# Kernel tuning notes

Measured on AMD Instinct MI355X. Metric: run time of the kernel, lower is better.

Reference implementation:

```python
import jax, jax.numpy as jnp
import numpy as np

N = 32768          # flattened tokens
D = 256            # latent_dim
K = 8192           # codebook_size
COMMIT_W = 0.25    # commitment_weight


def setup_inputs() -> dict:
    key = jax.random.key(0)
    k1, k2, k3 = jax.random.split(key, 3)
    x = jax.random.normal(k1, (N, D), dtype=jnp.float32)
    # nn.init.uniform_(embedding.weight, -1/K, 1/K)
    embedding = jax.random.uniform(k2, (K, D), dtype=jnp.float32,
                                   minval=-1.0 / K, maxval=1.0 / K)
    # out_proj: Linear(D, D, bias=False); torch default kaiming-uniform ~ U(-1/sqrt(D), 1/sqrt(D))
    lim = 1.0 / np.sqrt(D)
    w_out = jax.random.uniform(k3, (D, D), dtype=jnp.float32, minval=-lim, maxval=lim)
    return {"x": x, "embedding": embedding, "w_out": w_out}


def reference(x, embedding, w_out):
    sg = jax.lax.stop_gradient
    # codebook = out_proj(embedding.weight)  -> [K, D]
    codebook = embedding @ w_out.T
    # torch.cdist(x, codebook, p=2) is only consumed by argmin, so squared
    # Euclidean distances give the identical ids without the sqrt.
    x2 = jnp.sum(x * x, axis=1, keepdims=True)          # [N, 1]
    c2 = jnp.sum(codebook * codebook, axis=1)           # [K]
    dists = x2 - 2.0 * (x @ codebook.T) + c2            # [N, K]
    ids = jnp.argmin(dists, axis=1)                     # [N]
    q = codebook[ids]                                   # [N, D] gather
    # straight-through estimator
    quantized = x + sg(q - x)
    loss = jnp.mean((x - sg(quantized)) ** 2) \
         + COMMIT_W * jnp.mean((quantized - sg(x)) ** 2)
    return quantized, ids, loss
```

## Files before the change

kernel.cpp:

```cpp
#include <hip/hip_runtime.h>
#include <hip/hip_bf16.h>

#define N_TOK 32768
#define DIM   256
#define KCB   8192
#define CAP   64
#define MARGIN 1.75e-4f

typedef __attribute__((ext_vector_type(8))) short short8v;
typedef __attribute__((ext_vector_type(4))) float f32x4;

__device__ __forceinline__ unsigned int mono_f32(float f) {
    unsigned int u = __float_as_uint(f);
    return (u >> 31) ? ~u : (u | 0x80000000u);
}
__device__ __forceinline__ float invmono_f32(unsigned int m) {
    unsigned int u = (m & 0x80000000u) ? (m & 0x7FFFFFFFu) : ~m;
    return __uint_as_float(u);
}
__device__ __forceinline__ unsigned long long shfl_xor_u64(unsigned long long v, int m) {
    unsigned int lo = (unsigned int)v, hi = (unsigned int)(v >> 32);
    lo = __shfl_xor(lo, m, 64);
    hi = __shfl_xor(hi, m, 64);
    return ((unsigned long long)hi << 32) | lo;
}
__device__ __forceinline__ void gl_lds16(const void* g, void* l) {
    __builtin_amdgcn_global_load_lds(
        (const __attribute__((address_space(1))) unsigned int*)g,
        (__attribute__((address_space(3))) unsigned int*)l, 16, 0, 0);
}
__device__ __forceinline__ unsigned int rne16(float f) {
    unsigned int b = __float_as_uint(f);
    return (b + 0x7FFFu + ((b >> 16) & 1u)) >> 16;
}

__global__ __launch_bounds__(256) void transpose_w(const float* __restrict__ w,
                                                   float* __restrict__ wT) {
    __shared__ float tile[32][33];
    int bx = blockIdx.x & 7, by = blockIdx.x >> 3;
    int x0 = bx * 32, y0 = by * 32;
    int tx = threadIdx.x & 31, ty = threadIdx.x >> 5;
    #pragma unroll
    for (int i = 0; i < 32; i += 8)
        tile[ty + i][tx] = w[(y0 + ty + i) * DIM + x0 + tx];
    __syncthreads();
    #pragma unroll
    for (int i = 0; i < 32; i += 8)
        wT[(x0 + ty + i) * DIM + y0 + tx] = tile[tx][ty + i];
}

#define KPB 8
__global__ __launch_bounds__(256) void build_codebook(const float* __restrict__ emb,
                                                      const float* __restrict__ wT,
                                                      float* __restrict__ cb) {
    __shared__ float e[KPB][DIM];
    const int k0 = blockIdx.x * KPB;
    const int t = threadIdx.x;
    for (int i = t; i < KPB * DIM / 4; i += 256)
        ((float4*)&e[0][0])[i] = ((const float4*)(emb + (size_t)k0 * DIM))[i];
    __syncthreads();
    const int d = t;
    float acc[KPB];
    #pragma unroll
    for (int kk = 0; kk < KPB; ++kk) acc[kk] = 0.f;
    for (int j = 0; j < DIM; ++j) {
        float w = wT[j * DIM + d];
        #pragma unroll
        for (int kk = 0; kk < KPB; ++kk)
            acc[kk] = fmaf(e[kk][j], w, acc[kk]);
    }
    #pragma unroll
    for (int kk = 0; kk < KPB; ++kk)
        cb[(size_t)(k0 + kk) * DIM + d] = acc[kk];
}

__global__ __launch_bounds__(256) void sumsq_np_bf(const float* __restrict__ a,
                                                   float* __restrict__ out,
                                                   uint4* __restrict__ bfout) {
    #pragma clang fp contract(off)
    int idx = blockIdx.x * 256 + threadIdx.x;
    int r = idx >> 1, h = idx & 1;
    const float* b = a + (size_t)r * DIM + h * 128;
    uint4* dst = bfout ? bfout + ((size_t)r * 32 + h * 16) : (uint4*)0;
    float r0 = 0.f, r1 = 0.f, r2 = 0.f, r3 = 0.f,
          r4 = 0.f, r5 = 0.f, r6 = 0.f, r7 = 0.f;
    #pragma unroll
    for (int i = 0; i < 128; i += 8) {
        float4 p = *(const float4*)(b + i);
        float4 q = *(const float4*)(b + i + 4);
        if (bfout) {
            uint4 u;
            u.x = rne16(p.x) | (rne16(p.y) << 16);
            u.y = rne16(p.z) | (rne16(p.w) << 16);
            u.z = rne16(q.x) | (rne16(q.y) << 16);
            u.w = rne16(q.z) | (rne16(q.w) << 16);
            dst[i >> 3] = u;
        }
        r0 = r0 + p.x * p.x; r1 = r1 + p.y * p.y;
        r2 = r2 + p.z * p.z; r3 = r3 + p.w * p.w;
        r4 = r4 + q.x * q.x; r5 = r5 + q.y * q.y;
        r6 = r6 + q.z * q.z; r7 = r7 + q.w * q.w;
    }
    float half = ((r0 + r1) + (r2 + r3)) + ((r4 + r5) + (r6 + r7));
    float other = __shfl_xor(half, 1, 64);
    if (h == 0) out[r] = half + other;
}

__global__ __launch_bounds__(512, 2) void score_collect(
    const unsigned short* __restrict__ xbf,
    const unsigned short* __restrict__ cbbf,
    unsigned int* __restrict__ gmax,
    unsigned int* __restrict__ ccnt,
    unsigned short* __restrict__ cand)
{
    __shared__ unsigned char lds[131072];
    __shared__ float auxm[2][256];
    const int t = threadIdx.x;
    const int l = t & 63, w = t >> 6;
    const int g = l >> 4, c = l & 15;
    const int wr = w >> 1, wc = w & 1;
    const int bid = blockIdx.x;
    const int bx = (bid & 7) + 8 * ((bid >> 3) & 15);
    const int by = bid >> 7;
    const int row0 = bx * 256;
    const int col0 = by * 256;

    f32x4 acc[4][8];
    #pragma unroll
    for (int m = 0; m < 4; ++m)
        #pragma unroll
        for (int n = 0; n < 8; ++n) acc[m][n] = (f32x4){0.f, 0.f, 0.f, 0.f};

    const char* xg = (const char*)xbf  + (size_t)row0 * 512;
    const char* cg = (const char*)cbbf + (size_t)col0 * 512;

#define STAGE(buf, ks)                                                         \
    do {                                                                       \
        const int kb_ = (ks) * 128;                                            \
        unsigned char* la_ = lds + (buf) * 65536;                              \
        _Pragma("unroll")                                                      \
        for (int r_ = 0; r_ < 4; ++r_) {            \
            int i_ = r_ * 512 + t;                                             \
            int row_ = i_ >> 3, pc_ = i_ & 7;                                  \
            gl_lds16(xg + (size_t)row_ * 512 + kb_ + ((pc_ ^ (row_ & 7)) * 16),\
                     la_ + i_ * 16);                                           \
        }                                                                      \
        _Pragma("unroll")                                                      \
        for (int r_ = 0; r_ < 4; ++r_) {            \
            int i_ = r_ * 512 + t;                                             \
            int row_ = i_ >> 3, pc_ = i_ & 7;                                  \
            gl_lds16(cg + (size_t)row_ * 512 + kb_ + ((pc_ ^ (row_ & 7)) * 16),\
                     la_ + 32768 + i_ * 16);                                   \
        }                                                                      \
    } while (0)

#define COMPUTE(buf)                                                           \
    do {                                                                       \
        const unsigned char* la_ = lds + (buf) * 65536;                        \
        const unsigned char* lb_ = la_ + 32768;                                \
        _Pragma("unroll")                                                      \
        for (int kk = 0; kk < 2; ++kk) {                                       \
            const int sw_ = ((kk * 4 + g) ^ (c & 7)) * 16;                     \
            short8v af[4], bv[8];                                              \
            _Pragma("unroll")                                                  \
            for (int m = 0; m < 4; ++m)                                        \
                af[m] = *(const short8v*)(la_ + (64 * wr + 16 * m + c) * 128 + sw_); \
            _Pragma("unroll")                                                  \
            for (int n = 0; n < 8; ++n)                                        \
                bv[n] = *(const short8v*)(lb_ + (128 * wc + 16 * n + c) * 128 + sw_); \
            _Pragma("unroll")                                                  \
            for (int m = 0; m < 4; ++m)                                        \
                _Pragma("unroll")                                              \
                for (int n = 0; n < 8; ++n)                                    \
                    acc[m][n] = __builtin_amdgcn_mfma_f32_16x16x32_bf16(       \
                        af[m], bv[n], acc[m][n], 0, 0, 0);                     \
        }                                                                      \
    } while (0)

    STAGE(0, 0); STAGE(1, 1);
    asm volatile("s_waitcnt vmcnt(8)" ::: "memory");
    __builtin_amdgcn_s_barrier();
    asm volatile("" ::: "memory");

    COMPUTE(0);
    __builtin_amdgcn_s_barrier();
    asm volatile("" ::: "memory");
    STAGE(0, 2);
    asm volatile("s_waitcnt vmcnt(8)" ::: "memory");
    __builtin_amdgcn_s_barrier();
    asm volatile("" ::: "memory");

    COMPUTE(1);
    __builtin_amdgcn_s_barrier();
    asm volatile("" ::: "memory");
    STAGE(1, 3);
    asm volatile("s_waitcnt vmcnt(8)" ::: "memory");
    __builtin_amdgcn_s_barrier();
    asm volatile("" ::: "memory");

    COMPUTE(0);
    asm volatile("s_waitcnt vmcnt(0)" ::: "memory");
    __builtin_amdgcn_s_barrier();
    asm volatile("" ::: "memory");

    COMPUTE(1);
#undef STAGE
#undef COMPUTE

    #pragma unroll
    for (int m = 0; m < 4; ++m)
        #pragma unroll
        for (int j = 0; j < 4; ++j) {
            float v = acc[m][0][j];
            #pragma unroll
            for (int n = 1; n < 8; ++n) v = fmaxf(v, acc[m][n][j]);
            #pragma unroll
            for (int msk = 1; msk < 16; msk <<= 1)
                v = fmaxf(v, __shfl_xor(v, msk, 64));
            if (c == 0) auxm[wc][64 * wr + 16 * m + 4 * g + j] = v;
        }
    __syncthreads();

    if (wc == 0 && c == 0) {
        float vm[16];
        unsigned int ou[16];
        #pragma unroll
        for (int i = 0; i < 16; ++i) {
            int row = 64 * wr + 16 * (i >> 2) + 4 * g + (i & 3);
            vm[i] = fmaxf(auxm[0][row], auxm[1][row]);
        }
        #pragma unroll
        for (int i = 0; i < 16; ++i) {
            int row = 64 * wr + 16 * (i >> 2) + 4 * g + (i & 3);
            ou[i] = atomicMax(&gmax[row0 + row], mono_f32(vm[i]));
        }
        #pragma unroll
        for (int i = 0; i < 16; ++i) {
            int row = 64 * wr + 16 * (i >> 2) + 4 * g + (i & 3);
            auxm[0][row] = fmaxf(vm[i], invmono_f32(ou[i]));
        }
    }
    __syncthreads();

    #pragma unroll
    for (int m = 0; m < 4; ++m)
        #pragma unroll
        for (int j = 0; j < 4; ++j) {
            int lrow = 64 * wr + 16 * m + 4 * g + j;
            float thr = auxm[0][lrow] - MARGIN;
            #pragma unroll
            for (int n = 0; n < 8; ++n) {
                float s = acc[m][n][j];
                if (s >= thr) {
                    int row = row0 + lrow;
                    unsigned int idx = atomicAdd(&ccnt[row], 1u);
                    if (idx < CAP)
                        cand[((size_t)row << 6) + idx] =
                            (unsigned short)(col0 + 128 * wc + 16 * n + c);
                }
            }
        }
}

__device__ __forceinline__ unsigned long long np_dist_pack(
    const float4* __restrict__ xr4, const float* __restrict__ cb,
    int k, float X2, const float* __restrict__ c2)
{
    #pragma clang fp contract(off)
    const float4* cr4 = (const float4*)(cb + (size_t)k * DIM);
    float a = 0.f;
    #pragma unroll 8
    for (int t4 = 0; t4 < DIM / 4; ++t4) {
        float4 xv = xr4[t4];
        float4 cv = cr4[t4];
        a = fmaf(xv.x, cv.x, a);
        a = fmaf(xv.y, cv.y, a);
        a = fmaf(xv.z, cv.z, a);
        a = fmaf(xv.w, cv.w, a);
    }
    float u  = X2 - 2.0f * a;
    float dd = u + c2[k];
    return ((unsigned long long)mono_f32(dd) << 32) | (unsigned int)k;
}

__global__ __launch_bounds__(256) void exact_select(
    const float* __restrict__ x, const float* __restrict__ cb,
    const float* __restrict__ x2, const float* __restrict__ c2,
    const unsigned int* __restrict__ ccnt, const unsigned short* __restrict__ cand,
    unsigned long long* __restrict__ best)
{
    const int l = threadIdx.x & 63;
    const int row = (blockIdx.x * 256 + threadIdx.x) >> 6;
    const unsigned int cnt = ccnt[row];
    const float4* xr4 = (const float4*)(x + (size_t)row * DIM);
    const float X2 = x2[row];
    unsigned long long bp = ~0ull;

    if (cnt <= CAP) {
        if (l < (int)cnt) {
            int k = (int)cand[((size_t)row << 6) + l];
            bp = np_dist_pack(xr4, cb, k, X2, c2);
        }
    } else {
        for (int k = l; k < KCB; k += 64) {
            unsigned long long pk = np_dist_pack(xr4, cb, k, X2, c2);
            if (pk < bp) bp = pk;
        }
    }
    #pragma unroll
    for (int m = 1; m < 64; m <<= 1) {
        unsigned long long v = shfl_xor_u64(bp, m);
        if (v < bp) bp = v;
    }
    if (l == 0) best[row] = bp;
}

__global__ __launch_bounds__(256, 4) void score_argmin(const float* __restrict__ x,
                                                       const float* __restrict__ cb,
                                                       const float* __restrict__ c2,
                                                       const float* __restrict__ x2,
                                                       unsigned long long* __restrict__ best) {
    #pragma clang fp contract(off)
    __shared__ float As[16][128];
    __shared__ float Bs[16][128];
    const int row0 = blockIdx.x * 128;
    const int col0 = blockIdx.y * 128;
    const int t = threadIdx.x;
    const int tn = t & 15, tm = t >> 4;
    const int lrow = t >> 1, lseg = (t & 1) * 4;
    float acc[8][8];
    #pragma unroll
    for (int i = 0; i < 8; ++i)
        #pragma unroll
        for (int j = 0; j < 8; ++j) acc[i][j] = 0.f;
    const float* xp = x  + (size_t)(row0 + lrow) * DIM + lseg;
    const float* cp = cb + (size_t)(col0 + lrow) * DIM + lseg;
    for (int k0 = 0; k0 < DIM; k0 += 16) {
        float4 a0 = *(const float4*)(xp + k0);
        float4 a1 = *(const float4*)(xp + k0 + 8);
        float4 b0 = *(const float4*)(cp + k0);
        float4 b1 = *(const float4*)(cp + k0 + 8);
        __syncthreads();
        As[lseg + 0][lrow] = a0.x; As[lseg + 1][lrow] = a0.y;
        As[lseg + 2][lrow] = a0.z; As[lseg + 3][lrow] = a0.w;
        As[8 + lseg + 0][lrow] = a1.x; As[8 + lseg + 1][lrow] = a1.y;
        As[8 + lseg + 2][lrow] = a1.z; As[8 + lseg + 3][lrow] = a1.w;
        Bs[lseg + 0][lrow] = b0.x; Bs[lseg + 1][lrow] = b0.y;
        Bs[lseg + 2][lrow] = b0.z; Bs[lseg + 3][lrow] = b0.w;
        Bs[8 + lseg + 0][lrow] = b1.x; Bs[8 + lseg + 1][lrow] = b1.y;
        Bs[8 + lseg + 2][lrow] = b1.z; Bs[8 + lseg + 3][lrow] = b1.w;
        __syncthreads();
        #pragma unroll
        for (int kk = 0; kk < 16; ++kk) {
            float a[8], b[8];
            *(float4*)(a)     = *(const float4*)&As[kk][tm * 4];
            *(float4*)(a + 4) = *(const float4*)&As[kk][64 + tm * 4];
            *(float4*)(b)     = *(const float4*)&Bs[kk][tn * 4];
            *(float4*)(b + 4) = *(const float4*)&Bs[kk][64 + tn * 4];
            #pragma unroll
            for (int i = 0; i < 8; ++i)
                #pragma unroll
                for (int j = 0; j < 8; ++j)
                    acc[i][j] = fmaf(a[i], b[j], acc[i][j]);
        }
    }
    float c2v[8], x2v[8];
    #pragma unroll
    for (int j = 0; j < 4; ++j) {
        c2v[j]     = c2[col0 + tn * 4 + j];
        c2v[4 + j] = c2[col0 + 64 + tn * 4 + j];
    }
    #pragma unroll
    for (int i = 0; i < 4; ++i) {
        x2v[i]     = x2[row0 + tm * 4 + i];
        x2v[4 + i] = x2[row0 + 64 + tm * 4 + i];
    }
    #pragma unroll
    for (int i = 0; i < 8; ++i) {
        unsigned long long bp = ~0ull;
        #pragma unroll
        for (int j = 0; j < 8; ++j) {
            float tt = 2.0f * acc[i][j];
            float u  = x2v[i] - tt;
            float dd = u + c2v[j];
            int id = col0 + ((j < 4) ? (tn * 4 + j) : (64 + tn * 4 + (j - 4)));
            unsigned long long pk = ((unsigned long long)mono_f32(dd) << 32) | (unsigned int)id;
            if (pk < bp) bp = pk;
        }
        #pragma unroll
        for (int m = 1; m < 16; m <<= 1) {
            unsigned long long v = shfl_xor_u64(bp, m);
            if (v < bp) bp = v;
        }
        if (tn == 0) {
            int gr = row0 + ((i < 4) ? (tm * 4 + i) : (64 + tm * 4 + (i - 4)));
            atomicMin(&best[gr], bp);
        }
    }
}

__global__ __launch_bounds__(256) void finalize(const float* __restrict__ x,
                                                const float* __restrict__ cb,
                                                const unsigned long long* __restrict__ best,
                                                float* __restrict__ out,
                                                float* __restrict__ partial) {
    __shared__ float rsum[16];
    const int t = threadIdx.x;
    const int rloc = t >> 4, seg = t & 15;
    const int r = blockIdx.x * 16 + rloc;
    const int id = (int)(best[r] & 0xFFFFFFFFu);
    const float4* xp = (const float4*)(x  + (size_t)r  * DIM) + seg * 4;
    const float4* cp = (const float4*)(cb + (size_t)id * DIM) + seg * 4;
    float4*       op = (float4*)(out + (size_t)r * DIM) + seg * 4;
    float s = 0.f;
    #pragma unroll
    for (int i = 0; i < 4; ++i) {
        float4 xv = xp[i], qv = cp[i];
        op[i] = qv;
        float dx = xv.x - qv.x, dy = xv.y - qv.y;
        float dz = xv.z - qv.z, dw = xv.w - qv.w;
        s += dx * dx + dy * dy + dz * dz + dw * dw;
    }
    #pragma unroll
    for (int m = 1; m < 16; m <<= 1) s += __shfl_xor(s, m, 64);
    if (seg == 0) {
        rsum[rloc] = s;
        out[(size_t)N_TOK * DIM + r] = (float)id;
    }
    __syncthreads();
    if (t == 0) {
        float bs = 0.f;
        #pragma unroll
        for (int i = 0; i < 16; ++i) bs += rsum[i];
        partial[blockIdx.x] = bs;
    }
}

__global__ __launch_bounds__(256) void reduce_loss(const float* __restrict__ partial,
                                                   float* __restrict__ out) {
    float s = 0.f;
    for (int i = threadIdx.x; i < 2048 / 4; i += 256) {
        float4 v = ((const float4*)partial)[i];
        s += (v.x + v.y) + (v.z + v.w);
    }
    #pragma unroll
    for (int o = 32; o > 0; o >>= 1) s += __shfl_down(s, o, 64);
    __shared__ float w4[4];
    if ((threadIdx.x & 63) == 0) w4[threadIdx.x >> 6] = s;
    __syncthreads();
    if (threadIdx.x == 0)
        out[(size_t)N_TOK * DIM + N_TOK] =
            (w4[0] + w4[1] + w4[2] + w4[3]) * (1.25f / ((float)N_TOK * (float)DIM));
}

extern "C" void kernel_launch(void* const* d_in, const int* in_sizes, int n_in,
                              void* d_out, int out_size, void* d_ws, size_t ws_size,
                              hipStream_t stream) {
    const float* x     = (const float*)d_in[0];
    const float* emb   = (const float*)d_in[1];
    const float* w_out = (const float*)d_in[2];
    float* out = (float*)d_out;

    char* ws = (char*)d_ws;
    unsigned long long* best = (unsigned long long*)ws;
    float* x2 = (float*)(ws + 262400);
    float* wT = (float*)(ws + 393472);
    float* cb = (float*)(ws + 655616);
    float* c2 = (float*)(ws + 9044224);
    unsigned int*   gmax = (unsigned int*)(ws + 9076992);
    unsigned int*   ccnt = (unsigned int*)(ws + 9208064);
    unsigned short* cand = (unsigned short*)(ws + 9339136);
    unsigned short* xbf  = (unsigned short*)(ws + 13533440);
    unsigned short* cbbf = (unsigned short*)(ws + 30310656);
    float* partial = wT;
    const size_t NEED = 34504960;
    const bool useMfma = (ws_size >= NEED);

    transpose_w   <<<64,  256, 0, stream>>>(w_out, wT);
    build_codebook<<<KCB / KPB, 256, 0, stream>>>(emb, wT, cb);
    sumsq_np_bf   <<<N_TOK * 2 / 256, 256, 0, stream>>>(x, x2,
                      useMfma ? (uint4*)xbf : (uint4*)0);
    sumsq_np_bf   <<<KCB * 2 / 256, 256, 0, stream>>>(cb, c2,
                      useMfma ? (uint4*)cbbf : (uint4*)0);

    if (useMfma) {
        hipMemsetAsync(gmax, 0, 262144, stream);
        score_collect <<<4096, 512, 0, stream>>>(xbf, cbbf, gmax, ccnt, cand);
        exact_select  <<<N_TOK / 4, 256, 0, stream>>>(x, cb, x2, c2, ccnt, cand, best);
    } else {
        hipMemsetAsync(best, 0xFF, 262144, stream);
        score_argmin  <<<dim3(N_TOK / 128, KCB / 128), 256, 0, stream>>>(x, cb, c2, x2, best);
    }

    finalize      <<<N_TOK / 16, 256, 0, stream>>>(x, cb, best, out, partial);
    reduce_loss   <<<1, 256, 0, stream>>>(partial, out);
}
```

Before: 514.7 us.

## Pipeline score GEMM at half-K granularity with interleaved staging and MFMA priority

```diff
diff --git a/kernel.cpp b/kernel.cpp
--- a/kernel.cpp
+++ b/kernel.cpp
@@ -113,8 +113,8 @@
     unsigned int* __restrict__ ccnt,
     unsigned short* __restrict__ cand)
 {
-    __shared__ unsigned char lds[131072];
-    __shared__ float auxm[2][256];
+    __shared__ unsigned char lds[133120];
+    float* auxm = (float*)(lds + 131072);
     const int t = threadIdx.x;
     const int l = t & 63, w = t >> 6;
     const int g = l >> 4, c = l & 15;
@@ -133,80 +133,137 @@
 
     const char* xg = (const char*)xbf  + (size_t)row0 * 512;
     const char* cg = (const char*)cbbf + (size_t)col0 * 512;
-
-#define STAGE(buf, ks)                                                         \
+    short8v af[4], bv[4];
+    const int swq = ((g ^ (c & 3) ^ ((c >> 2) & 3)) & 3) * 16;
+
+#define ASL(p2_, kkh_) ((p2_) * 32768 + (kkh_) * 16384)
+#define BSL(p2_, kkh_) (65536 + (p2_) * 32768 + (kkh_) * 16384)
+
+#define STG(ptr_, slot_, s_, kkh_)                                             \
     do {                                                                       \
-        const int kb_ = (ks) * 128;                                            \
-        unsigned char* la_ = lds + (buf) * 65536;                              \
         _Pragma("unroll")                                                      \
-        for (int r_ = 0; r_ < 4; ++r_) {            \
+        for (int r_ = 0; r_ < 2; ++r_) {                                       \
             int i_ = r_ * 512 + t;                                             \
-            int row_ = i_ >> 3, pc_ = i_ & 7;                                  \
-            gl_lds16(xg + (size_t)row_ * 512 + kb_ + ((pc_ ^ (row_ & 7)) * 16),\
-                     la_ + i_ * 16);                                           \
-        }                                                                      \
-        _Pragma("unroll")                                                      \
-        for (int r_ = 0; r_ < 4; ++r_) {            \
-            int i_ = r_ * 512 + t;                                             \
-            int row_ = i_ >> 3, pc_ = i_ & 7;                                  \
-            gl_lds16(cg + (size_t)row_ * 512 + kb_ + ((pc_ ^ (row_ & 7)) * 16),\
-                     la_ + 32768 + i_ * 16);                                   \
+            int row_ = i_ >> 2, pc_ = i_ & 3;                                  \
+            int sz_ = (row_ ^ (row_ >> 2)) & 3;                                \
+            gl_lds16((ptr_) + (size_t)row_ * 512 + (s_) * 128 + (kkh_) * 64    \
+                             + ((pc_ ^ sz_) * 16),                             \
+                     lds + (slot_) + i_ * 16);                                 \
         }                                                                      \
     } while (0)
 
-#define COMPUTE(buf)                                                           \
+#define RDA(slot_)                                                             \
     do {                                                                       \
-        const unsigned char* la_ = lds + (buf) * 65536;                        \
-        const unsigned char* lb_ = la_ + 32768;                                \
+        const unsigned char* ap_ = lds + (slot_);                              \
         _Pragma("unroll")                                                      \
-        for (int kk = 0; kk < 2; ++kk) {                                       \
-            const int sw_ = ((kk * 4 + g) ^ (c & 7)) * 16;                     \
-            short8v af[4], bv[8];                                              \
+        for (int m = 0; m < 4; ++m)                                            \
+            af[m] = *(const short8v*)(ap_ + (64 * wr + 16 * m + c) * 64 + swq);\
+    } while (0)
+
+#define RDB(slot_, nh_)                                                        \
+    do {                                                                       \
+        const unsigned char* bp_ = lds + (slot_);                              \
+        _Pragma("unroll")                                                      \
+        for (int j = 0; j < 4; ++j)                                            \
+            bv[j] = *(const short8v*)(bp_ +                                    \
+                (128 * wc + 16 * ((nh_) * 4 + j) + c) * 64 + swq);             \
+    } while (0)
+
+#define MM(nh_)                                                                \
+    do {                                                                       \
+        __builtin_amdgcn_s_setprio(1);                                         \
+        _Pragma("unroll")                                                      \
+        for (int m = 0; m < 4; ++m)                                            \
             _Pragma("unroll")                                                  \
-            for (int m = 0; m < 4; ++m)                                        \
-                af[m] = *(const short8v*)(la_ + (64 * wr + 16 * m + c) * 128 + sw_); \
-            _Pragma("unroll")                                                  \
-            for (int n = 0; n < 8; ++n)                                        \
-                bv[n] = *(const short8v*)(lb_ + (128 * wc + 16 * n + c) * 128 + sw_); \
-            _Pragma("unroll")                                                  \
-            for (int m = 0; m < 4; ++m)                                        \
-                _Pragma("unroll")                                              \
-                for (int n = 0; n < 8; ++n)                                    \
-                    acc[m][n] = __builtin_amdgcn_mfma_f32_16x16x32_bf16(       \
-                        af[m], bv[n], acc[m][n], 0, 0, 0);                     \
-        }                                                                      \
+            for (int j = 0; j < 4; ++j)                                        \
+                acc[m][(nh_) * 4 + j] = __builtin_amdgcn_mfma_f32_16x16x32_bf16(\
+                    af[m], bv[j], acc[m][(nh_) * 4 + j], 0, 0, 0);             \
+        __builtin_amdgcn_s_setprio(0);                                         \
     } while (0)
 
-    STAGE(0, 0); STAGE(1, 1);
-    asm volatile("s_waitcnt vmcnt(8)" ::: "memory");
-    __builtin_amdgcn_s_barrier();
-    asm volatile("" ::: "memory");
-
-    COMPUTE(0);
-    __builtin_amdgcn_s_barrier();
-    asm volatile("" ::: "memory");
-    STAGE(0, 2);
-    asm volatile("s_waitcnt vmcnt(8)" ::: "memory");
-    __builtin_amdgcn_s_barrier();
-    asm volatile("" ::: "memory");
-
-    COMPUTE(1);
-    __builtin_amdgcn_s_barrier();
-    asm volatile("" ::: "memory");
-    STAGE(1, 3);
-    asm volatile("s_waitcnt vmcnt(8)" ::: "memory");
-    __builtin_amdgcn_s_barrier();
-    asm volatile("" ::: "memory");
-
-    COMPUTE(0);
-    asm volatile("s_waitcnt vmcnt(0)" ::: "memory");
-    __builtin_amdgcn_s_barrier();
-    asm volatile("" ::: "memory");
-
-    COMPUTE(1);
-#undef STAGE
-#undef COMPUTE
-
+#define BAR() do { __builtin_amdgcn_s_barrier(); asm volatile("" ::: "memory"); } while (0)
+#define WV6() asm volatile("s_waitcnt vmcnt(6)" ::: "memory")
+#define WV4() asm volatile("s_waitcnt vmcnt(4)" ::: "memory")
+#define WV0() asm volatile("s_waitcnt vmcnt(0)" ::: "memory")
+
+    STG(xg, ASL(0, 0), 0, 0);
+    STG(cg, BSL(0, 0), 0, 0);
+    STG(xg, ASL(0, 1), 0, 1);
+    STG(cg, BSL(0, 1), 0, 1);
+    STG(xg, ASL(1, 0), 1, 0);
+    WV6(); BAR();
+
+    RDA(ASL(0, 0)); RDB(BSL(0, 0), 0);
+    STG(cg, BSL(1, 0), 1, 0); STG(xg, ASL(1, 1), 1, 1);
+    MM(0);
+    WV6(); BAR();
+    RDB(BSL(0, 0), 1);
+    STG(cg, BSL(1, 1), 1, 1);
+    MM(1);
+    BAR();
+    RDA(ASL(0, 1)); RDB(BSL(0, 1), 0);
+    STG(xg, ASL(0, 0), 2, 0);
+    MM(0);
+    BAR();
+    RDB(BSL(0, 1), 1);
+    MM(1);
+
+    WV6(); BAR();
+    RDA(ASL(1, 0)); RDB(BSL(1, 0), 0);
+    STG(cg, BSL(0, 0), 2, 0); STG(xg, ASL(0, 1), 2, 1);
+    MM(0);
+    WV6(); BAR();
+    RDB(BSL(1, 0), 1);
+    STG(cg, BSL(0, 1), 2, 1);
+    MM(1);
+    BAR();
+    RDA(ASL(1, 1)); RDB(BSL(1, 1), 0);
+    STG(xg, ASL(1, 0), 3, 0);
+    MM(0);
+    BAR();
+    RDB(BSL(1, 1), 1);
+    MM(1);
+
+    WV6(); BAR();
+    RDA(ASL(0, 0)); RDB(BSL(0, 0), 0);
+    STG(cg, BSL(1, 0), 3, 0); STG(xg, ASL(1, 1), 3, 1);
+    MM(0);
+    WV6(); BAR();
+    RDB(BSL(0, 0), 1);
+    STG(cg, BSL(1, 1), 3, 1);
+    MM(1);
+    BAR();
+    RDA(ASL(0, 1)); RDB(BSL(0, 1), 0);
+    MM(0);
+    BAR();
+    RDB(BSL(0, 1), 1);
+    MM(1);
+
+    WV4(); BAR();
+    RDA(ASL(1, 0)); RDB(BSL(1, 0), 0);
+    MM(0);
+    WV0(); BAR();
+    RDB(BSL(1, 0), 1);
+    MM(1);
+    BAR();
+    RDA(ASL(1, 1)); RDB(BSL(1, 1), 0);
+    MM(0);
+    BAR();
+    RDB(BSL(1, 1), 1);
+    MM(1);
+
+#undef STG
+#undef RDA
+#undef RDB
+#undef MM
+#undef BAR
+#undef WV6
+#undef WV4
+#undef WV0
+#undef ASL
+#undef BSL
+
+    __syncthreads();
     #pragma unroll
     for (int m = 0; m < 4; ++m)
         #pragma unroll
@@ -217,7 +274,7 @@
             #pragma unroll
             for (int msk = 1; msk < 16; msk <<= 1)
                 v = fmaxf(v, __shfl_xor(v, msk, 64));
-            if (c == 0) auxm[wc][64 * wr + 16 * m + 4 * g + j] = v;
+            if (c == 0) auxm[wc * 256 + 64 * wr + 16 * m + 4 * g + j] = v;
         }
     __syncthreads();
 
@@ -227,7 +284,7 @@
         #pragma unroll
         for (int i = 0; i < 16; ++i) {
             int row = 64 * wr + 16 * (i >> 2) + 4 * g + (i & 3);
-            vm[i] = fmaxf(auxm[0][row], auxm[1][row]);
+            vm[i] = fmaxf(auxm[row], auxm[256 + row]);
         }
         #pragma unroll
         for (int i = 0; i < 16; ++i) {
@@ -237,7 +294,7 @@
         #pragma unroll
         for (int i = 0; i < 16; ++i) {
             int row = 64 * wr + 16 * (i >> 2) + 4 * g + (i & 3);
-            auxm[0][row] = fmaxf(vm[i], invmono_f32(ou[i]));
+            auxm[row] = fmaxf(vm[i], invmono_f32(ou[i]));
         }
     }
     __syncthreads();
@@ -247,7 +304,7 @@
         #pragma unroll
         for (int j = 0; j < 4; ++j) {
             int lrow = 64 * wr + 16 * m + 4 * g + j;
-            float thr = auxm[0][lrow] - MARGIN;
+            float thr = auxm[lrow] - MARGIN;
             #pragma unroll
             for (int n = 0; n < 8; ++n) {
                 float s = acc[m][n][j];
```

After: 531.7 us. 3.3% more time.

## Restructure score_collect to 16 waves with smaller K-slices and loop pipeline

Applied to the files above, without the earlier changes.

```diff
diff --git a/kernel.cpp b/kernel.cpp
--- a/kernel.cpp
+++ b/kernel.cpp
@@ -106,104 +106,83 @@
     if (h == 0) out[r] = half + other;
 }
 
-__global__ __launch_bounds__(512, 2) void score_collect(
+__global__ __launch_bounds__(1024, 4) void score_collect(
     const unsigned short* __restrict__ xbf,
     const unsigned short* __restrict__ cbbf,
     unsigned int* __restrict__ gmax,
     unsigned int* __restrict__ ccnt,
     unsigned short* __restrict__ cand)
 {
-    __shared__ unsigned char lds[131072];
-    __shared__ float auxm[2][256];
+    __shared__ unsigned char lds[69632];
+    float* auxm = (float*)(lds + 65536);
     const int t = threadIdx.x;
     const int l = t & 63, w = t >> 6;
     const int g = l >> 4, c = l & 15;
-    const int wr = w >> 1, wc = w & 1;
+    const int wr = w >> 2, wc = w & 3;
     const int bid = blockIdx.x;
     const int bx = (bid & 7) + 8 * ((bid >> 3) & 15);
     const int by = bid >> 7;
     const int row0 = bx * 256;
     const int col0 = by * 256;
 
-    f32x4 acc[4][8];
+    f32x4 acc[4][4];
     #pragma unroll
     for (int m = 0; m < 4; ++m)
         #pragma unroll
-        for (int n = 0; n < 8; ++n) acc[m][n] = (f32x4){0.f, 0.f, 0.f, 0.f};
+        for (int n = 0; n < 4; ++n) acc[m][n] = (f32x4){0.f, 0.f, 0.f, 0.f};
 
     const char* xg = (const char*)xbf  + (size_t)row0 * 512;
     const char* cg = (const char*)cbbf + (size_t)col0 * 512;
 
 #define STAGE(buf, ks)                                                         \
     do {                                                                       \
-        const int kb_ = (ks) * 128;                                            \
-        unsigned char* la_ = lds + (buf) * 65536;                              \
-        _Pragma("unroll")                                                      \
-        for (int r_ = 0; r_ < 4; ++r_) {            \
-            int i_ = r_ * 512 + t;                                             \
-            int row_ = i_ >> 3, pc_ = i_ & 7;                                  \
-            gl_lds16(xg + (size_t)row_ * 512 + kb_ + ((pc_ ^ (row_ & 7)) * 16),\
-                     la_ + i_ * 16);                                           \
+        const int kb_ = (ks) * 64;                                             \
+        unsigned char* la_ = lds + (buf) * 32768;                              \
+        {                  \
+            int row_ = t >> 2, pc_ = t & 3;                                    \
+            int sz_ = (row_ >> 1) & 3;                                         \
+            gl_lds16(xg + (size_t)row_ * 512 + kb_ + ((pc_ ^ sz_) * 16),       \
+                     la_ + t * 16);                                            \
         }                                                                      \
-        _Pragma("unroll")                                                      \
-        for (int r_ = 0; r_ < 4; ++r_) {            \
-            int i_ = r_ * 512 + t;                                             \
-            int row_ = i_ >> 3, pc_ = i_ & 7;                                  \
-            gl_lds16(cg + (size_t)row_ * 512 + kb_ + ((pc_ ^ (row_ & 7)) * 16),\
-                     la_ + 32768 + i_ * 16);                                   \
+        {                                          \
+            int row_ = t >> 2, pc_ = t & 3;                                    \
+            int sz_ = (row_ >> 1) & 3;                                         \
+            gl_lds16(cg + (size_t)row_ * 512 + kb_ + ((pc_ ^ sz_) * 16),       \
+                     la_ + 16384 + t * 16);                                    \
         }                                                                      \
     } while (0)
 
 #define COMPUTE(buf)                                                           \
     do {                                                                       \
-        const unsigned char* la_ = lds + (buf) * 65536;                        \
-        const unsigned char* lb_ = la_ + 32768;                                \
+        const unsigned char* la_ = lds + (buf) * 32768;                        \
+        const unsigned char* lb_ = la_ + 16384;                                \
+        const int swq_ = (g ^ ((c >> 1) & 3)) * 16;                            \
+        short8v af[4], bv[4];                                                  \
         _Pragma("unroll")                                                      \
-        for (int kk = 0; kk < 2; ++kk) {                                       \
-            const int sw_ = ((kk * 4 + g) ^ (c & 7)) * 16;                     \
-            short8v af[4], bv[8];                                              \
+        for (int m = 0; m < 4; ++m)                                            \
+            af[m] = *(const short8v*)(la_ + (64 * wr + 16 * m + c) * 64 + swq_); \
+        _Pragma("unroll")                                                      \
+        for (int n = 0; n < 4; ++n)                                            \
+            bv[n] = *(const short8v*)(lb_ + (64 * wc + 16 * n + c) * 64 + swq_); \
+        _Pragma("unroll")                                                      \
+        for (int m = 0; m < 4; ++m)                                            \
             _Pragma("unroll")                                                  \
-            for (int m = 0; m < 4; ++m)                                        \
-                af[m] = *(const short8v*)(la_ + (64 * wr + 16 * m + c) * 128 + sw_); \
-            _Pragma("unroll")                                                  \
-            for (int n = 0; n < 8; ++n)                                        \
-                bv[n] = *(const short8v*)(lb_ + (128 * wc + 16 * n + c) * 128 + sw_); \
-            _Pragma("unroll")                                                  \
-            for (int m = 0; m < 4; ++m)                                        \
-                _Pragma("unroll")                                              \
-                for (int n = 0; n < 8; ++n)                                    \
-                    acc[m][n] = __builtin_amdgcn_mfma_f32_16x16x32_bf16(       \
-                        af[m], bv[n], acc[m][n], 0, 0, 0);                     \
-        }                                                                      \
+            for (int n = 0; n < 4; ++n)                                        \
+                acc[m][n] = __builtin_amdgcn_mfma_f32_16x16x32_bf16(           \
+                    af[m], bv[n], acc[m][n], 0, 0, 0);                         \
     } while (0)
 
-    STAGE(0, 0); STAGE(1, 1);
-    asm volatile("s_waitcnt vmcnt(8)" ::: "memory");
-    __builtin_amdgcn_s_barrier();
-    asm volatile("" ::: "memory");
-
-    COMPUTE(0);
-    __builtin_amdgcn_s_barrier();
-    asm volatile("" ::: "memory");
-    STAGE(0, 2);
-    asm volatile("s_waitcnt vmcnt(8)" ::: "memory");
-    __builtin_amdgcn_s_barrier();
-    asm volatile("" ::: "memory");
-
-    COMPUTE(1);
-    __builtin_amdgcn_s_barrier();
-    asm volatile("" ::: "memory");
-    STAGE(1, 3);
-    asm volatile("s_waitcnt vmcnt(8)" ::: "memory");
-    __builtin_amdgcn_s_barrier();
-    asm volatile("" ::: "memory");
-
-    COMPUTE(0);
+    STAGE(0, 0);
     asm volatile("s_waitcnt vmcnt(0)" ::: "memory");
-    __builtin_amdgcn_s_barrier();
-    asm volatile("" ::: "memory");
-
-    COMPUTE(1);
+    __syncthreads();
+
+    #pragma unroll
+    for (int s = 0; s < 8; ++s) {
+        if (s < 7) STAGE((s + 1) & 1, s + 1);
+        COMPUTE(s & 1);
+        asm volatile("s_waitcnt vmcnt(0)" ::: "memory");
+        __syncthreads();
+    }
 #undef STAGE
 #undef COMPUTE
 
@@ -213,32 +192,19 @@
         for (int j = 0; j < 4; ++j) {
             float v = acc[m][0][j];
             #pragma unroll
-            for (int n = 1; n < 8; ++n) v = fmaxf(v, acc[m][n][j]);
+            for (int n = 1; n < 4; ++n) v = fmaxf(v, acc[m][n][j]);
             #pragma unroll
             for (int msk = 1; msk < 16; msk <<= 1)
                 v = fmaxf(v, __shfl_xor(v, msk, 64));
-            if (c == 0) auxm[wc][64 * wr + 16 * m + 4 * g + j] = v;
-        }
-    __syncthreads();
-
-    if (wc == 0 && c == 0) {
-        float vm[16];
-        unsigned int ou[16];
-        #pragma unroll
-        for (int i = 0; i < 16; ++i) {
-            int row = 64 * wr + 16 * (i >> 2) + 4 * g + (i & 3);
-            vm[i] = fmaxf(auxm[0][row], auxm[1][row]);
-        }
-        #pragma unroll
-        for (int i = 0; i < 16; ++i) {
-            int row = 64 * wr + 16 * (i >> 2) + 4 * g + (i & 3);
-            ou[i] = atomicMax(&gmax[row0 + row], mono_f32(vm[i]));
-        }
-        #pragma unroll
-        for (int i = 0; i < 16; ++i) {
-            int row = 64 * wr + 16 * (i >> 2) + 4 * g + (i & 3);
-            auxm[0][row] = fmaxf(vm[i], invmono_f32(ou[i]));
-        }
+            if (c == 0) auxm[wc * 256 + 64 * wr + 16 * m + 4 * g + j] = v;
+        }
+    __syncthreads();
+
+    if (t < 256) {
+        float vm = fmaxf(fmaxf(auxm[t], auxm[256 + t]),
+                         fmaxf(auxm[512 + t], auxm[768 + t]));
+        unsigned int ou = atomicMax(&gmax[row0 + t], mono_f32(vm));
+        auxm[t] = fmaxf(vm, invmono_f32(ou));
     }
     __syncthreads();
 
@@ -247,16 +213,16 @@
         #pragma unroll
         for (int j = 0; j < 4; ++j) {
             int lrow = 64 * wr + 16 * m + 4 * g + j;
-            float thr = auxm[0][lrow] - MARGIN;
+            float thr = auxm[lrow] - MARGIN;
             #pragma unroll
-            for (int n = 0; n < 8; ++n) {
+            for (int n = 0; n < 4; ++n) {
                 float s = acc[m][n][j];
                 if (s >= thr) {
                     int row = row0 + lrow;
                     unsigned int idx = atomicAdd(&ccnt[row], 1u);
                     if (idx < CAP)
                         cand[((size_t)row << 6) + idx] =
-                            (unsigned short)(col0 + 128 * wc + 16 * n + c);
+                            (unsigned short)(col0 + 64 * wc + 16 * n + c);
                 }
             }
         }
@@ -485,7 +451,7 @@
 
     if (useMfma) {
         hipMemsetAsync(gmax, 0, 262144, stream);
-        score_collect <<<4096, 512, 0, stream>>>(xbf, cbbf, gmax, ccnt, cand);
+        score_collect <<<4096, 1024, 0, stream>>>(xbf, cbbf, gmax, ccnt, cand);
         exact_select  <<<N_TOK / 4, 256, 0, stream>>>(x, cb, x2, c2, ccnt, cand, best);
     } else {
         hipMemsetAsync(best, 0xFF, 262144, stream);
```

New measurement: 471.3 us. 8.4% less time.
